# Performance work log

Hardware: AMD Instinct MI355X
Metric: run time of the kernel (lower is better)

## Reference

```python
import jax, jax.numpy as jnp
import numpy as np

EMB = 1024
HEADS = 16
DH = EMB // HEADS
EPS = 1e-5


def setup_inputs() -> dict:
    key = jax.random.key(0)
    ks = jax.random.split(key, 8)
    s = 0.02
    return {
        "x": jax.random.normal(ks[0], (4, 2048, EMB), dtype=jnp.float32),
        "Wq": jax.random.normal(ks[1], (EMB, EMB), dtype=jnp.float32) * s,
        "Wk": jax.random.normal(ks[2], (EMB, EMB), dtype=jnp.float32) * s,
        "Wv": jax.random.normal(ks[3], (EMB, EMB), dtype=jnp.float32) * s,
        "Wo": jax.random.normal(ks[4], (EMB, EMB), dtype=jnp.float32) * s,
        "bo": jnp.zeros((EMB,), dtype=jnp.float32),
        "W1": jax.random.normal(ks[5], (EMB, 4 * EMB), dtype=jnp.float32) * s,
        "b1": jnp.zeros((4 * EMB,), dtype=jnp.float32),
        "W2": jax.random.normal(ks[6], (4 * EMB, EMB), dtype=jnp.float32) * s,
        "b2": jnp.zeros((EMB,), dtype=jnp.float32),
        "g1": jnp.ones((EMB,), dtype=jnp.float32),
        "beta1": jnp.zeros((EMB,), dtype=jnp.float32),
        "g2": jnp.ones((EMB,), dtype=jnp.float32),
        "beta2": jnp.zeros((EMB,), dtype=jnp.float32),
    }


def _layernorm(x, scale, bias):
    mean = jnp.mean(x, axis=-1, keepdims=True)
    var = jnp.mean((x - mean) ** 2, axis=-1, keepdims=True)  # unbiased=False
    return scale * ((x - mean) / jnp.sqrt(var + EPS)) + bias


def _attention(x, Wq, Wk, Wv, Wo, bo):
    B, S, _ = x.shape
    q = (x @ Wq).reshape(B, S, HEADS, DH).transpose(0, 2, 1, 3)  # b h s d
    k = (x @ Wk).reshape(B, S, HEADS, DH).transpose(0, 2, 1, 3)
    v = (x @ Wv).reshape(B, S, HEADS, DH).transpose(0, 2, 1, 3)
    scores = jnp.einsum("bhqd,bhkd->bhqk", q, k)
    causal = jnp.tril(jnp.ones((S, S), dtype=bool))
    scores = jnp.where(causal, scores, -jnp.inf)
    w = jax.nn.softmax(scores / jnp.sqrt(jnp.float32(DH)), axis=-1)
    ctx = jnp.einsum("bhqk,bhkd->bhqd", w, v).transpose(0, 2, 1, 3).reshape(B, S, HEADS * DH)
    return ctx @ Wo + bo


def reference(x, Wq, Wk, Wv, Wo, bo, W1, b1, W2, b2, g1, beta1, g2, beta2):
    # pre-LN attention + residual
    h = x + _attention(_layernorm(x, g1, beta1), Wq, Wk, Wv, Wo, bo)
    # pre-LN FFN (exact GELU, as torch nn.GELU default) + residual
    y = _layernorm(h, g2, beta2)
    y = jax.nn.gelu(y @ W1 + b1, approximate=False) @ W2 + b2
    return h + y
```

## Files before the change

### kernel.cpp

```cpp
#include <hip/hip_runtime.h>
#include <hip/hip_bf16.h>

#define EMB 1024
#define SEQ 2048
#define BATCH 4
#define TOK (BATCH*SEQ)
#define NH 16
#define DH 64
#define FF 4096

typedef unsigned short u16;
typedef __bf16 bf16x8 __attribute__((ext_vector_type(8)));
typedef float f32x4 __attribute__((ext_vector_type(4)));

union frag_u { uint4 u4; bf16x8 bf; u16 us[8]; };

__device__ __forceinline__ u16 f2bf(float f) {
  union { float f; unsigned u; } a; a.f = f;
  unsigned r = a.u + 0x7fffu + ((a.u >> 16) & 1u);
  return (u16)(r >> 16);
}
__device__ __forceinline__ float bf2f(u16 u) {
  union { unsigned u; float f; } a; a.u = ((unsigned)u) << 16; return a.f;
}
__device__ __forceinline__ unsigned cvt_pk_bf16(float lo, float hi) {
  unsigned r;
  asm("v_cvt_pk_bf16_f32 %0, %1, %2" : "=v"(r) : "v"(lo), "v"(hi));
  return r;
}
__device__ __forceinline__ float exp2_hw(float x) {
  float r;
  asm("v_exp_f32 %0, %1" : "=v"(r) : "v"(x));
  return r;
}

__device__ __forceinline__ void glds16(const void* g, void* l) {
  __builtin_amdgcn_global_load_lds((const __attribute__((address_space(1))) void*)g,
                                   (__attribute__((address_space(3))) void*)l, 16, 0, 0);
}

__device__ __forceinline__ float gelu_fast(float u) {
  float u2 = u * u;
  float c = fmaf(u2, 0.0356774081f, 0.7978845608f);
  float e = __expf(2.f * u * c);
  return u * e * __builtin_amdgcn_rcpf(e + 1.f);
}

__device__ __forceinline__ void cvt_t_body(const float* __restrict__ src,
                                           u16* __restrict__ dst,
                                           int N, int ldk, int bx, int by) {
  __shared__ float tile[32][33];
  int c0 = bx * 32, r0 = by * 32;
  int tc = threadIdx.x & 31, tr = threadIdx.x >> 5;
  #pragma unroll
  for (int p = 0; p < 4; p++)
    tile[tr + p * 8][tc] = src[(size_t)(r0 + tr + p * 8) * N + c0 + tc];
  __syncthreads();
  #pragma unroll
  for (int p = 0; p < 4; p++)
    dst[(size_t)(c0 + tr + p * 8) * ldk + r0 + tc] = f2bf(tile[tc][tr + p * 8]);
}

__global__ __launch_bounds__(256) void prep_kernel(const float* Wq, const float* Wk,
                                                   const float* Wv, const float* Wo,
                                                   const float* W1, const float* W2,
                                                   u16* wqkv_t, u16* wo_t,
                                                   u16* w1_t, u16* w2_t) {
  int id = blockIdx.x;
  if (id < 4096) {
    const float* s = (id < 1024) ? Wq : (id < 2048) ? Wk : (id < 3072) ? Wv : Wo;
    u16* d = (id < 1024) ? wqkv_t : (id < 2048) ? wqkv_t + 1024 * 1024
           : (id < 3072) ? wqkv_t + 2 * 1024 * 1024 : wo_t;
    int local = id & 1023;
    cvt_t_body(s, d, 1024, 1024, local & 31, local >> 5);
  } else if (id < 8192) {
    int local = id - 4096;
    cvt_t_body(W1, w1_t, 4096, 1024, local & 127, local >> 7);
  } else {
    int local = id - 8192;
    cvt_t_body(W2, w2_t, 1024, 4096, local & 31, local >> 5);
  }
}

template <int IN_BF16>
__global__ __launch_bounds__(256) void ln_kernel(const void* __restrict__ xv,
                                                 const float* __restrict__ g,
                                                 const float* __restrict__ be,
                                                 u16* __restrict__ out) {
  int wave = threadIdx.x >> 6, lane = threadIdx.x & 63;
  int row = blockIdx.x * 4 + wave;
  float v[16];
  float s = 0.f;
  if (IN_BF16) {
    const u16* xr = (const u16*)xv + (size_t)row * EMB;
    #pragma unroll
    for (int i = 0; i < 4; i++) {
      ushort4 u = *(const ushort4*)(xr + i * 256 + lane * 4);
      v[i * 4 + 0] = bf2f(u.x); v[i * 4 + 1] = bf2f(u.y);
      v[i * 4 + 2] = bf2f(u.z); v[i * 4 + 3] = bf2f(u.w);
      s += v[i * 4] + v[i * 4 + 1] + v[i * 4 + 2] + v[i * 4 + 3];
    }
  } else {
    const float* xr = (const float*)xv + (size_t)row * EMB;
    #pragma unroll
    for (int i = 0; i < 4; i++) {
      float4 u = *(const float4*)(xr + i * 256 + lane * 4);
      v[i * 4 + 0] = u.x; v[i * 4 + 1] = u.y; v[i * 4 + 2] = u.z; v[i * 4 + 3] = u.w;
      s += u.x + u.y + u.z + u.w;
    }
  }
  #pragma unroll
  for (int m = 1; m < 64; m <<= 1) s += __shfl_xor(s, m, 64);
  float mean = s * (1.f / EMB);
  float vs = 0.f;
  #pragma unroll
  for (int i = 0; i < 16; i++) { float dx = v[i] - mean; vs += dx * dx; }
  #pragma unroll
  for (int m = 1; m < 64; m <<= 1) vs += __shfl_xor(vs, m, 64);
  float inv = rsqrtf(vs * (1.f / EMB) + 1e-5f);
  u16* orow = out + (size_t)row * EMB;
  #pragma unroll
  for (int i = 0; i < 4; i++) {
    int c = i * 256 + lane * 4;
    float4 gv = *(const float4*)(g + c);
    float4 bv = *(const float4*)(be + c);
    ushort4 o;
    o.x = f2bf(gv.x * (v[i * 4 + 0] - mean) * inv + bv.x);
    o.y = f2bf(gv.y * (v[i * 4 + 1] - mean) * inv + bv.y);
    o.z = f2bf(gv.z * (v[i * 4 + 2] - mean) * inv + bv.z);
    o.w = f2bf(gv.w * (v[i * 4 + 3] - mean) * inv + bv.w);
    *(ushort4*)(orow + c) = o;
  }
}

template <int MODE>
__global__ __launch_bounds__(512) void gemm256(const u16* __restrict__ A,
                                               const u16* __restrict__ Bt,
                                               const float* __restrict__ bias,
                                               void* __restrict__ outp,
                                               int N, int K) {
  __shared__ __align__(16) u16 As[256 * 64];
  __shared__ __align__(16) u16 Bs[128 * 64];
  const int t = threadIdx.x;
  const int w = t >> 6, lane = t & 63;
  const int l15 = lane & 15, quad = lane >> 4;
  const int wr = w >> 1, wc = w & 1;

  const int gx = gridDim.x;
  const int nwg = gx * gridDim.y;
  const int id0 = blockIdx.y * gx + blockIdx.x;
  const int nid = (id0 & 7) * (nwg >> 3) + (id0 >> 3);
  const int rowBase = (nid / gx) * 256, colBase = (nid % gx) * 128;

  const int sr = lane >> 3;
  const int sc = ((lane & 7) ^ sr) * 8;
  const u16* gA = A + (size_t)(rowBase + w * 8 + sr) * K + sc;
  const u16* gB = Bt + (size_t)(colBase + w * 8 + sr) * K + sc;
  u16* lA = As + w * 8 * 64;
  u16* lB = Bs + w * 8 * 64;

  const int swz0 = (quad ^ (l15 & 7)) * 8;
  const int swz1 = ((quad + 4) ^ (l15 & 7)) * 8;

  f32x4 zero = {0.f, 0.f, 0.f, 0.f};
  f32x4 acc[4][4];
  #pragma unroll
  for (int i = 0; i < 4; i++)
    #pragma unroll
    for (int j = 0; j < 4; j++) acc[i][j] = zero;

  for (int k0 = 0; k0 < K; k0 += 64) {
    __syncthreads();
    #pragma unroll
    for (int j = 0; j < 4; j++)
      glds16(gA + (size_t)(j * 64) * K + k0, lA + j * 64 * 64);
    #pragma unroll
    for (int j = 0; j < 2; j++)
      glds16(gB + (size_t)(j * 64) * K + k0, lB + j * 64 * 64);
    __syncthreads();
    #pragma unroll
    for (int kk = 0; kk < 2; kk++) {
      const int so = kk ? swz1 : swz0;
      frag_u a4[4], b4[4];
      #pragma unroll
      for (int mi = 0; mi < 4; mi++)
        a4[mi].u4 = *(const uint4*)(As + (wr * 64 + mi * 16 + l15) * 64 + so);
      #pragma unroll
      for (int ni = 0; ni < 4; ni++)
        b4[ni].u4 = *(const uint4*)(Bs + (wc * 64 + ni * 16 + l15) * 64 + so);
      #pragma unroll
      for (int mi = 0; mi < 4; mi++)
        #pragma unroll
        for (int ni = 0; ni < 4; ni++)
          acc[mi][ni] = __builtin_amdgcn_mfma_f32_16x16x32_bf16(a4[mi].bf, b4[ni].bf, acc[mi][ni], 0, 0, 0);
    }
  }

  #pragma unroll
  for (int mi = 0; mi < 4; mi++) {
    #pragma unroll
    for (int ni = 0; ni < 4; ni++) {
      int col = colBase + wc * 64 + ni * 16 + l15;
      int row0 = rowBase + wr * 64 + mi * 16 + quad * 4;
      if (MODE == 1) {
        int mat = col >> 10, cc = col & 1023;
        int hh = cc >> 6, d = cc & 63;
        int b = row0 >> 11, s0 = row0 & 2047;
        if (mat == 2) {
          uint2 pk;
          pk.x = (unsigned)f2bf(acc[mi][ni][0]) | ((unsigned)f2bf(acc[mi][ni][1]) << 16);
          pk.y = (unsigned)f2bf(acc[mi][ni][2]) | ((unsigned)f2bf(acc[mi][ni][3]) << 16);
          *(uint2*)((u16*)outp + 2 * (size_t)TOK * EMB +
                    ((size_t)((b * NH + hh) * DH + d)) * SEQ + s0) = pk;
        } else {
          const float m = (mat == 0) ? 0.1803368801f : 1.f;
          #pragma unroll
          for (int r = 0; r < 4; r++)
            ((u16*)outp)[(size_t)mat * (TOK * EMB) +
                         (((size_t)(b * NH + hh) * SEQ + s0 + r) << 6) + d] = f2bf(acc[mi][ni][r] * m);
        }
      } else {
        #pragma unroll
        for (int r = 0; r < 4; r++) {
          float vv = gelu_fast(acc[mi][ni][r] + bias[col]);
          ((u16*)outp)[(size_t)(row0 + r) * N + col] = f2bf(vv);
        }
      }
    }
  }
}

template <int MODE>
__global__ __launch_bounds__(256) void gemm128(const u16* __restrict__ A,
                                               const u16* __restrict__ Bt,
                                               const float* __restrict__ bias,
                                               const void* __restrict__ resid,
                                               void* __restrict__ outp,
                                               int N, int K) {
  __shared__ __align__(16) u16 As[2][128 * 64];
  __shared__ __align__(16) u16 Bs[2][128 * 64];
  const int t = threadIdx.x;
  const int w = t >> 6, lane = t & 63;
  const int l15 = lane & 15, quad = lane >> 4;
  const int wr = w >> 1, wc = w & 1;

  const int gx = gridDim.x;
  const int nwg = gx * gridDim.y;
  const int id0 = blockIdx.y * gx + blockIdx.x;
  const int nid = (id0 & 7) * (nwg >> 3) + (id0 >> 3);
  const int rowBase = (nid / gx) * 128, colBase = (nid % gx) * 128;

  const int sr = lane >> 3;
  const int sc = ((lane & 7) ^ sr) * 8;
  const u16* gA = A + (size_t)(rowBase + w * 8 + sr) * K + sc;
  const u16* gB = Bt + (size_t)(colBase + w * 8 + sr) * K + sc;
  const int ldsOff = (w * 8) * 64;

  const int swz0 = (quad ^ (l15 & 7)) * 8;
  const int swz1 = ((quad + 4) ^ (l15 & 7)) * 8;

  f32x4 zero = {0.f, 0.f, 0.f, 0.f};
  f32x4 acc[4][4];
  #pragma unroll
  for (int i = 0; i < 4; i++)
    #pragma unroll
    for (int j = 0; j < 4; j++) acc[i][j] = zero;

  const int nt = K >> 6;
  #pragma unroll
  for (int j = 0; j < 4; j++) {
    glds16(gA + (size_t)(j * 32) * K, As[0] + ldsOff + j * 32 * 64);
    glds16(gB + (size_t)(j * 32) * K, Bs[0] + ldsOff + j * 32 * 64);
  }
  #pragma unroll
  for (int j = 0; j < 4; j++) {
    glds16(gA + (size_t)(j * 32) * K + 64, As[1] + ldsOff + j * 32 * 64);
    glds16(gB + (size_t)(j * 32) * K + 64, Bs[1] + ldsOff + j * 32 * 64);
  }

  for (int tt = 0; tt < nt; tt++) {
    const int cur = tt & 1;
    if (tt + 1 < nt) asm volatile("s_waitcnt vmcnt(8)" ::: "memory");
    else             asm volatile("s_waitcnt vmcnt(0)" ::: "memory");
    __builtin_amdgcn_sched_barrier(0);
    __builtin_amdgcn_s_barrier();

    const u16* as = As[cur];
    const u16* bs = Bs[cur];
    #pragma unroll
    for (int kk = 0; kk < 2; kk++) {
      const int so = kk ? swz1 : swz0;
      frag_u a4[4], b4[4];
      #pragma unroll
      for (int mi = 0; mi < 4; mi++)
        a4[mi].u4 = *(const uint4*)(as + (wr * 64 + mi * 16 + l15) * 64 + so);
      #pragma unroll
      for (int ni = 0; ni < 4; ni++)
        b4[ni].u4 = *(const uint4*)(bs + (wc * 64 + ni * 16 + l15) * 64 + so);
      __builtin_amdgcn_s_setprio(1);
      #pragma unroll
      for (int mi = 0; mi < 4; mi++)
        #pragma unroll
        for (int ni = 0; ni < 4; ni++)
          acc[mi][ni] = __builtin_amdgcn_mfma_f32_16x16x32_bf16(a4[mi].bf, b4[ni].bf, acc[mi][ni], 0, 0, 0);
      __builtin_amdgcn_s_setprio(0);
    }
    asm volatile("s_waitcnt lgkmcnt(0)" ::: "memory");
    __builtin_amdgcn_sched_barrier(0);
    __builtin_amdgcn_s_barrier();

    if (tt + 2 < nt) {
      const int k0 = (tt + 2) << 6;
      #pragma unroll
      for (int j = 0; j < 4; j++) {
        glds16(gA + (size_t)(j * 32) * K + k0, As[cur] + ldsOff + j * 32 * 64);
        glds16(gB + (size_t)(j * 32) * K + k0, Bs[cur] + ldsOff + j * 32 * 64);
      }
    }
  }

  #pragma unroll
  for (int mi = 0; mi < 4; mi++) {
    #pragma unroll
    for (int ni = 0; ni < 4; ni++) {
      int col = colBase + wc * 64 + ni * 16 + l15;
      int row0 = rowBase + wr * 64 + mi * 16 + quad * 4;
      #pragma unroll
      for (int r = 0; r < 4; r++) {
        int row = row0 + r;
        float vv = acc[mi][ni][r] + bias[col];
        if (MODE == 3) {
          vv += ((const float*)resid)[(size_t)row * N + col];
          ((u16*)outp)[(size_t)row * N + col] = f2bf(vv);
        } else {
          vv += bf2f(((const u16*)resid)[(size_t)row * N + col]);
          ((float*)outp)[(size_t)row * N + col] = vv;
        }
      }
    }
  }
}

__global__ __launch_bounds__(256) void attn_kernel(const u16* __restrict__ q,
                                                   const u16* __restrict__ k,
                                                   const u16* __restrict__ vt,
                                                   u16* __restrict__ ctx) {
  __shared__ __align__(16) u16 Ks[64 * 64];
  __shared__ __align__(16) u16 Vs[64 * 64];
  __shared__ __align__(16) u16 Ps[128 * 64];
  __shared__ float Ls[128];
  const int t = threadIdx.x;
  const int w = t >> 6, lane = t & 63;
  const int l15 = lane & 15, quad = lane >> 4;
  const int bh = blockIdx.x;
  const int qt = 15 - (int)blockIdx.y;
  const size_t base = (size_t)bh * SEQ * DH;
  const int bq = bh >> 4, hh = bh & 15;
  const int qBase = qt * 128;
  const int ktEnd = 2 * qt + 1;
  const int l7 = l15 & 7;

  const int r0 = w * 16 + (lane >> 3);
  const int scg = lane & 7;
  const int swzs = (scg ^ (r0 & 7)) * 8;
  const u16* gK = k + base + (size_t)r0 * DH + scg * 8;
  const u16* gV = vt + base + (size_t)r0 * SEQ + scg * 8;
  u16* sK0 = Ks + r0 * 64 + swzs;
  u16* sK1 = Ks + (r0 + 8) * 64 + swzs;
  u16* sV0 = Vs + r0 * 64 + swzs;
  u16* sV1 = Vs + (r0 + 8) * 64 + swzs;

  frag_u qf[2][2];
  #pragma unroll
  for (int ni = 0; ni < 2; ni++)
    #pragma unroll
    for (int ks = 0; ks < 2; ks++)
      qf[ni][ks].u4 = *(const uint4*)(q + base +
          (size_t)(qBase + w * 32 + ni * 16 + l15) * DH + ks * 32 + quad * 8);

  f32x4 zero = {0.f, 0.f, 0.f, 0.f};
  f32x4 oacc[2][4];
  #pragma unroll
  for (int mi = 0; mi < 2; mi++)
    #pragma unroll
    for (int n0 = 0; n0 < 4; n0++) oacc[mi][n0] = zero;
  float l0 = 0.f, l1 = 0.f;

  uint4 rK0 = *(const uint4*)(gK);
  uint4 rK1 = *(const uint4*)(gK + 8 * DH);
  uint4 rV0 = *(const uint4*)(gV);
  uint4 rV1 = *(const uint4*)(gV + (size_t)8 * SEQ);

  for (int kt = 0; kt <= ktEnd; kt++) {
    __syncthreads();
    *(uint4*)sK0 = rK0; *(uint4*)sK1 = rK1;
    *(uint4*)sV0 = rV0; *(uint4*)sV1 = rV1;
    __syncthreads();
    if (kt < ktEnd) {
      const int no = (kt + 1) * 64;
      rK0 = *(const uint4*)(gK + (size_t)no * DH);
      rK1 = *(const uint4*)(gK + (size_t)(no + 8) * DH);
      rV0 = *(const uint4*)(gV + no);
      rV1 = *(const uint4*)(gV + (size_t)8 * SEQ + no);
    }
    const int rel = kt - 2 * qt;
    if (rel == 1 && w < 2) continue;

    frag_u kf[4][2];
    #pragma unroll
    for (int mi = 0; mi < 4; mi++)
      #pragma unroll
      for (int ks = 0; ks < 2; ks++)
        kf[mi][ks].u4 = *(const uint4*)(Ks + (mi * 16 + l15) * 64 + (((ks * 4 + quad) ^ l7) * 8));
    f32x4 st[4][2];
    #pragma unroll
    for (int mi = 0; mi < 4; mi++)
      #pragma unroll
      for (int ni = 0; ni < 2; ni++) st[mi][ni] = zero;
    __builtin_amdgcn_s_setprio(1);
    #pragma unroll
    for (int ks = 0; ks < 2; ks++)
      #pragma unroll
      for (int mi = 0; mi < 4; mi++)
        #pragma unroll
        for (int ni = 0; ni < 2; ni++)
          st[mi][ni] = __builtin_amdgcn_mfma_f32_16x16x32_bf16(kf[mi][ks].bf, qf[ni][ks].bf, st[mi][ni], 0, 0, 0);
    __builtin_amdgcn_s_setprio(0);

    const bool doMask = (rel == 0 && w < 2) || (rel == 1);
    #pragma unroll
    for (int ni = 0; ni < 2; ni++) {
      const int qrow = qBase + w * 32 + ni * 16 + l15;
      float sum = 0.f;
      u16* prow = Ps + (w * 32 + ni * 16 + l15) * 64;
      #pragma unroll
      for (int mi = 0; mi < 4; mi++) {
        float p[4];
        if (doMask) {
          #pragma unroll
          for (int r = 0; r < 4; r++) {
            p[r] = exp2_hw(st[mi][ni][r]);
            if ((kt * 64 + mi * 16 + quad * 4 + r) > qrow) p[r] = 0.f;
            sum += p[r];
          }
        } else {
          #pragma unroll
          for (int r = 0; r < 4; r++) {
            p[r] = exp2_hw(st[mi][ni][r]);
            sum += p[r];
          }
        }
        uint2 pk;
        pk.x = cvt_pk_bf16(p[0], p[1]);
        pk.y = cvt_pk_bf16(p[2], p[3]);
        *(uint2*)(prow + (((mi * 2 + (quad >> 1)) ^ l7) * 8) + (quad & 1) * 4) = pk;
      }
      sum += __shfl_xor(sum, 16, 64);
      sum += __shfl_xor(sum, 32, 64);
      if (ni == 0) l0 += sum; else l1 += sum;
    }

    frag_u pa[2][2];
    #pragma unroll
    for (int mi = 0; mi < 2; mi++)
      #pragma unroll
      for (int ks = 0; ks < 2; ks++)
        pa[mi][ks].u4 = *(const uint4*)(Ps + (w * 32 + mi * 16 + l15) * 64 + (((ks * 4 + quad) ^ l7) * 8));
    __builtin_amdgcn_s_setprio(1);
    #pragma unroll
    for (int ks = 0; ks < 2; ks++)
      #pragma unroll
      for (int n0 = 0; n0 < 4; n0++) {
        frag_u b;
        b.u4 = *(const uint4*)(Vs + (n0 * 16 + l15) * 64 + (((ks * 4 + quad) ^ l7) * 8));
        #pragma unroll
        for (int mi = 0; mi < 2; mi++)
          oacc[mi][n0] = __builtin_amdgcn_mfma_f32_16x16x32_bf16(pa[mi][ks].bf, b.bf, oacc[mi][n0], 0, 0, 0);
      }
    __builtin_amdgcn_s_setprio(0);
  }

  if (quad == 0) {
    Ls[w * 32 + l15] = l0;
    Ls[w * 32 + 16 + l15] = l1;
  }
  #pragma unroll
  for (int mi = 0; mi < 2; mi++) {
    float il[4];
    #pragma unroll
    for (int r = 0; r < 4; r++) il[r] = 1.f / Ls[w * 32 + mi * 16 + quad * 4 + r];
    #pragma unroll
    for (int n0 = 0; n0 < 4; n0++) {
      int s = qBase + w * 32 + mi * 16 + quad * 4;
      int col = hh * 64 + n0 * 16 + l15;
      #pragma unroll
      for (int r = 0; r < 4; r++)
        ctx[((size_t)(bq * SEQ + s + r)) * EMB + col] = f2bf(oacc[mi][n0][r] * il[r]);
    }
  }
}

extern "C" void kernel_launch(void* const* d_in, const int* in_sizes, int n_in,
                              void* d_out, int out_size, void* d_ws, size_t ws_size,
                              hipStream_t stream) {
  const float* x  = (const float*)d_in[0];
  const float* Wq = (const float*)d_in[1];
  const float* Wk = (const float*)d_in[2];
  const float* Wv = (const float*)d_in[3];
  const float* Wo = (const float*)d_in[4];
  const float* bo = (const float*)d_in[5];
  const float* W1 = (const float*)d_in[6];
  const float* b1 = (const float*)d_in[7];
  const float* W2 = (const float*)d_in[8];
  const float* b2 = (const float*)d_in[9];
  const float* g1  = (const float*)d_in[10];
  const float* be1 = (const float*)d_in[11];
  const float* g2  = (const float*)d_in[12];
  const float* be2 = (const float*)d_in[13];
  float* out = (float*)d_out;
  char* ws = (char*)d_ws;
  const size_t MB = 1u << 20;

  u16* wqkv_t = (u16*)(ws + 0 * MB);
  u16* wo_t   = (u16*)(ws + 6 * MB);
  u16* w1_t   = (u16*)(ws + 8 * MB);
  u16* w2_t   = (u16*)(ws + 16 * MB);
  u16* hbuf   = (u16*)(ws + 24 * MB);
  u16* r1 = (u16*)(ws + 56 * MB);
  u16* qb = (u16*)(ws + 72 * MB);
  u16* f1 = (u16*)(ws + 72 * MB);

  prep_kernel<<<12288, 256, 0, stream>>>(Wq, Wk, Wv, Wo, W1, W2,
                                         wqkv_t, wo_t, w1_t, w2_t);

  ln_kernel<0><<<2048, 256, 0, stream>>>(x, g1, be1, r1);

  gemm256<1><<<dim3(24, 32), 512, 0, stream>>>(r1, wqkv_t, nullptr, qb, 3072, 1024);

  attn_kernel<<<dim3(64, 16), 256, 0, stream>>>(qb, qb + (size_t)TOK * EMB,
                                                qb + 2 * (size_t)TOK * EMB, r1);

  gemm128<3><<<dim3(8, 64), 256, 0, stream>>>(r1, wo_t, bo, x, hbuf, 1024, 1024);

  ln_kernel<1><<<2048, 256, 0, stream>>>(hbuf, g2, be2, r1);

  gemm256<2><<<dim3(32, 32), 512, 0, stream>>>(r1, w1_t, b1, f1, 4096, 1024);

  gemm128<4><<<dim3(8, 64), 256, 0, stream>>>(f1, w2_t, b2, hbuf, out, 1024, 4096);
}
```

Measured before the change: 436.3 us.

## Split-K the FFN2 GEMM into two halves with a separate reduce kernel

Replaces the single 512-block FFN2 GEMM (K=4096) with a split-K kernel that launches 1024 blocks, each computing half of K. One half's partial sums go to a workspace buffer and the other half's go straight into the output. A new elementwise kernel then adds the two partials, the bias and the residual. The aim is more parallelism and better CU occupancy for this long-K GEMM, at the cost of extra fp32 partial writes and reads plus an additional kernel launch. The new kernel also appears to drop the double-buffered LDS prefetch.

```diff
diff --git a/kernel.cpp b/kernel.cpp
--- a/kernel.cpp
+++ b/kernel.cpp
@@ -329,16 +329,108 @@
       for (int r = 0; r < 4; r++) {
         int row = row0 + r;
         float vv = acc[mi][ni][r] + bias[col];
-        if (MODE == 3) {
-          vv += ((const float*)resid)[(size_t)row * N + col];
-          ((u16*)outp)[(size_t)row * N + col] = f2bf(vv);
-        } else {
-          vv += bf2f(((const u16*)resid)[(size_t)row * N + col]);
-          ((float*)outp)[(size_t)row * N + col] = vv;
-        }
+        vv += ((const float*)resid)[(size_t)row * N + col];
+        ((u16*)outp)[(size_t)row * N + col] = f2bf(vv);
       }
     }
   }
+}
+
+__global__ __launch_bounds__(256) void gemm_sk(const u16* __restrict__ A,
+                                               const u16* __restrict__ Bt,
+                                               float* __restrict__ P0,
+                                               float* __restrict__ outp,
+                                               int N, int K) {
+  __shared__ __align__(16) u16 As[128 * 64];
+  __shared__ __align__(16) u16 Bs[128 * 64];
+  const int t = threadIdx.x;
+  const int w = t >> 6, lane = t & 63;
+  const int l15 = lane & 15, quad = lane >> 4;
+  const int wr = w >> 1, wc = w & 1;
+  const int z = blockIdx.z;
+  const int kBase = z * (K >> 1);
+  const int Kh = K >> 1;
+
+  const int gx = gridDim.x;
+  const int nwg = gx * gridDim.y;
+  const int id0 = blockIdx.y * gx + blockIdx.x;
+  const int nid = (id0 & 7) * (nwg >> 3) + (id0 >> 3);
+  const int rowBase = (nid / gx) * 128, colBase = (nid % gx) * 128;
+
+  const int sr = lane >> 3;
+  const int sc = ((lane & 7) ^ sr) * 8;
+  const u16* gA = A + (size_t)(rowBase + w * 8 + sr) * K + kBase + sc;
+  const u16* gB = Bt + (size_t)(colBase + w * 8 + sr) * K + kBase + sc;
+  u16* lA = As + (w * 8) * 64;
+  u16* lB = Bs + (w * 8) * 64;
+
+  const int swz0 = (quad ^ (l15 & 7)) * 8;
+  const int swz1 = ((quad + 4) ^ (l15 & 7)) * 8;
+
+  f32x4 zero = {0.f, 0.f, 0.f, 0.f};
+  f32x4 acc[4][4];
+  #pragma unroll
+  for (int i = 0; i < 4; i++)
+    #pragma unroll
+    for (int j = 0; j < 4; j++) acc[i][j] = zero;
+
+  for (int k0 = 0; k0 < Kh; k0 += 64) {
+    __syncthreads();
+    #pragma unroll
+    for (int j = 0; j < 4; j++) {
+      glds16(gA + (size_t)(j * 32) * K + k0, lA + j * 32 * 64);
+      glds16(gB + (size_t)(j * 32) * K + k0, lB + j * 32 * 64);
+    }
+    __syncthreads();
+    #pragma unroll
+    for (int kk = 0; kk < 2; kk++) {
+      const int so = kk ? swz1 : swz0;
+      frag_u a4[4], b4[4];
+      #pragma unroll
+      for (int mi = 0; mi < 4; mi++)
+        a4[mi].u4 = *(const uint4*)(As + (wr * 64 + mi * 16 + l15) * 64 + so);
+      #pragma unroll
+      for (int ni = 0; ni < 4; ni++)
+        b4[ni].u4 = *(const uint4*)(Bs + (wc * 64 + ni * 16 + l15) * 64 + so);
+      __builtin_amdgcn_s_setprio(1);
+      #pragma unroll
+      for (int mi = 0; mi < 4; mi++)
+        #pragma unroll
+        for (int ni = 0; ni < 4; ni++)
+          acc[mi][ni] = __builtin_amdgcn_mfma_f32_16x16x32_bf16(a4[mi].bf, b4[ni].bf, acc[mi][ni], 0, 0, 0);
+      __builtin_amdgcn_s_setprio(0);
+    }
+  }
+
+  float* dst = z ? outp : P0;
+  #pragma unroll
+  for (int mi = 0; mi < 4; mi++) {
+    #pragma unroll
+    for (int ni = 0; ni < 4; ni++) {
+      int col = colBase + wc * 64 + ni * 16 + l15;
+      int row0 = rowBase + wr * 64 + mi * 16 + quad * 4;
+      #pragma unroll
+      for (int r = 0; r < 4; r++)
+        dst[(size_t)(row0 + r) * N + col] = acc[mi][ni][r];
+    }
+  }
+}
+
+__global__ __launch_bounds__(256) void ffn2_reduce(float* __restrict__ outp,
+                                                   const float* __restrict__ P0,
+                                                   const float* __restrict__ bias,
+                                                   const u16* __restrict__ h) {
+  size_t i = ((size_t)blockIdx.x * 256 + threadIdx.x) * 4;
+  float4 o = *(float4*)(outp + i);
+  float4 p = *(const float4*)(P0 + i);
+  ushort4 hv = *(const ushort4*)(h + i);
+  int col = (int)(i & (EMB - 1));
+  float4 b = *(const float4*)(bias + col);
+  o.x += p.x + b.x + bf2f(hv.x);
+  o.y += p.y + b.y + bf2f(hv.y);
+  o.z += p.z + b.z + bf2f(hv.z);
+  o.w += p.w + b.w + bf2f(hv.w);
+  *(float4*)(outp + i) = o;
 }
 
 __global__ __launch_bounds__(256) void attn_kernel(const u16* __restrict__ q,
@@ -526,6 +618,7 @@
   u16* w1_t   = (u16*)(ws + 8 * MB);
   u16* w2_t   = (u16*)(ws + 16 * MB);
   u16* hbuf   = (u16*)(ws + 24 * MB);
+  float* p0   = (float*)(ws + 40 * MB);
   u16* r1 = (u16*)(ws + 56 * MB);
   u16* qb = (u16*)(ws + 72 * MB);
   u16* f1 = (u16*)(ws + 72 * MB);
@@ -546,5 +639,7 @@
 
   gemm256<2><<<dim3(32, 32), 512, 0, stream>>>(r1, w1_t, b1, f1, 4096, 1024);
 
-  gemm128<4><<<dim3(8, 64), 256, 0, stream>>>(f1, w2_t, b2, hbuf, out, 1024, 4096);
-}
+  gemm_sk<<<dim3(8, 64, 2), 256, 0, stream>>>(f1, w2_t, p0, out, 1024, 4096);
+
+  ffn2_reduce<<<(TOK * EMB) / (256 * 4), 256, 0, stream>>>(out, p0, b2, hbuf);
+}
```

Measured after the change: 481.4 us. +10.3%, slower.

## Double-buffer LDS tiles in GEMM with async prefetch two tiles ahead

Applied to the files above, without the earlier changes.

Moves the GEMM main loop to two LDS buffers per operand, so global-to-LDS loads for the next k-tiles are issued while MFMAs run on the current tile. Explicit vmcnt waits and raw s_barrier replace the pair of __syncthreads per iteration. MFMA blocks are wrapped in s_setprio to favour math issue. LDS usage doubles to 96KB per block, which may cut occupancy, and the hand-placed waitcnt values must match the number of outstanding loads for the result to stay correct.

```diff
diff --git a/kernel.cpp b/kernel.cpp
--- a/kernel.cpp
+++ b/kernel.cpp
@@ -139,8 +139,8 @@
                                                const float* __restrict__ bias,
                                                void* __restrict__ outp,
                                                int N, int K) {
-  __shared__ __align__(16) u16 As[256 * 64];
-  __shared__ __align__(16) u16 Bs[128 * 64];
+  __shared__ __align__(16) u16 As[2][256 * 64];
+  __shared__ __align__(16) u16 Bs[2][128 * 64];
   const int t = threadIdx.x;
   const int w = t >> 6, lane = t & 63;
   const int l15 = lane & 15, quad = lane >> 4;
@@ -156,8 +156,7 @@
   const int sc = ((lane & 7) ^ sr) * 8;
   const u16* gA = A + (size_t)(rowBase + w * 8 + sr) * K + sc;
   const u16* gB = Bt + (size_t)(colBase + w * 8 + sr) * K + sc;
-  u16* lA = As + w * 8 * 64;
-  u16* lB = Bs + w * 8 * 64;
+  const int ldsA = w * 8 * 64;
 
   const int swz0 = (quad ^ (l15 & 7)) * 8;
   const int swz1 = ((quad + 4) ^ (l15 & 7)) * 8;
@@ -169,30 +168,59 @@
     #pragma unroll
     for (int j = 0; j < 4; j++) acc[i][j] = zero;
 
-  for (int k0 = 0; k0 < K; k0 += 64) {
-    __syncthreads();
-    #pragma unroll
-    for (int j = 0; j < 4; j++)
-      glds16(gA + (size_t)(j * 64) * K + k0, lA + j * 64 * 64);
-    #pragma unroll
-    for (int j = 0; j < 2; j++)
-      glds16(gB + (size_t)(j * 64) * K + k0, lB + j * 64 * 64);
-    __syncthreads();
+  const int nt = K >> 6;
+  #pragma unroll
+  for (int j = 0; j < 4; j++)
+    glds16(gA + (size_t)(j * 64) * K, As[0] + ldsA + j * 64 * 64);
+  #pragma unroll
+  for (int j = 0; j < 2; j++)
+    glds16(gB + (size_t)(j * 64) * K, Bs[0] + ldsA + j * 64 * 64);
+  #pragma unroll
+  for (int j = 0; j < 4; j++)
+    glds16(gA + (size_t)(j * 64) * K + 64, As[1] + ldsA + j * 64 * 64);
+  #pragma unroll
+  for (int j = 0; j < 2; j++)
+    glds16(gB + (size_t)(j * 64) * K + 64, Bs[1] + ldsA + j * 64 * 64);
+
+  for (int tt = 0; tt < nt; tt++) {
+    const int cur = tt & 1;
+    if (tt + 1 < nt) asm volatile("s_waitcnt vmcnt(6)" ::: "memory");
+    else             asm volatile("s_waitcnt vmcnt(0)" ::: "memory");
+    __builtin_amdgcn_sched_barrier(0);
+    __builtin_amdgcn_s_barrier();
+
+    const u16* as = As[cur];
+    const u16* bs = Bs[cur];
     #pragma unroll
     for (int kk = 0; kk < 2; kk++) {
       const int so = kk ? swz1 : swz0;
       frag_u a4[4], b4[4];
       #pragma unroll
       for (int mi = 0; mi < 4; mi++)
-        a4[mi].u4 = *(const uint4*)(As + (wr * 64 + mi * 16 + l15) * 64 + so);
+        a4[mi].u4 = *(const uint4*)(as + (wr * 64 + mi * 16 + l15) * 64 + so);
       #pragma unroll
       for (int ni = 0; ni < 4; ni++)
-        b4[ni].u4 = *(const uint4*)(Bs + (wc * 64 + ni * 16 + l15) * 64 + so);
+        b4[ni].u4 = *(const uint4*)(bs + (wc * 64 + ni * 16 + l15) * 64 + so);
+      __builtin_amdgcn_s_setprio(1);
       #pragma unroll
       for (int mi = 0; mi < 4; mi++)
         #pragma unroll
         for (int ni = 0; ni < 4; ni++)
           acc[mi][ni] = __builtin_amdgcn_mfma_f32_16x16x32_bf16(a4[mi].bf, b4[ni].bf, acc[mi][ni], 0, 0, 0);
+      __builtin_amdgcn_s_setprio(0);
+    }
+    asm volatile("s_waitcnt lgkmcnt(0)" ::: "memory");
+    __builtin_amdgcn_sched_barrier(0);
+    __builtin_amdgcn_s_barrier();
+
+    if (tt + 2 < nt) {
+      const int k0 = (tt + 2) << 6;
+      #pragma unroll
+      for (int j = 0; j < 4; j++)
+        glds16(gA + (size_t)(j * 64) * K + k0, As[cur] + ldsA + j * 64 * 64);
+      #pragma unroll
+      for (int j = 0; j < 2; j++)
+        glds16(gB + (size_t)(j * 64) * K + k0, Bs[cur] + ldsA + j * 64 * 64);
     }
   }
 
```

After: 479.4 us. +9.9%, slower.
